# Performance work log

Hardware: AMD Instinct MI355X
Metric: run time of the kernel (lower is better)

Reference implementation:

```python
import jax, jax.numpy as jnp
import numpy as np

N, B, D_IN, D_OUT, E = 1024, 128, 64, 64, 16


def setup_inputs() -> dict:
    key = jax.random.key(0)
    k1, k2, k3, k4 = jax.random.split(key, 4)
    x = jax.random.normal(k1, (B, N, D_IN), dtype=jnp.float32)
    node_embeddings = jax.random.normal(k2, (N, E), dtype=jnp.float32)
    weights_pool = jax.random.normal(k3, (E, D_IN, D_OUT), dtype=jnp.float32)
    bias_pool = jax.random.normal(k4, (E, D_OUT), dtype=jnp.float32)
    return {"x": x, "node_embeddings": node_embeddings,
            "weights_pool": weights_pool, "bias_pool": bias_pool}


def reference(x, node_embeddings, weights_pool, bias_pool):
    # Adaptive adjacency: softmax over rows of relu(E E^T), shape [N, N]
    scores = jax.nn.relu(node_embeddings @ node_embeddings.T)
    supports = jax.nn.softmax(scores, axis=1)
    # Per-node weights [N, D_IN, D_OUT] and bias [N, D_OUT]
    weights = jnp.einsum('nd,dio->nio', node_embeddings, weights_pool)
    bias = node_embeddings @ bias_pool  # [N, D_OUT]
    # Graph aggregation: [B, N, D_IN]
    x_g = jnp.einsum('nm,bmc->bnc', supports, x)
    # Per-node linear transform + bias: [B, N, D_OUT]
    x_gconv = jnp.einsum('bni,nio->bno', x_g, weights) + bias
    return x_gconv
```

## Files before the change

kernel.cpp:

```cpp
#include <hip/hip_runtime.h>

#define N_NODES 1024
#define BATCH   128
#define E_DIM   16


typedef __attribute__((ext_vector_type(8))) short bf16x8;
typedef __attribute__((ext_vector_type(4))) float f32x4;
typedef __attribute__((ext_vector_type(16))) float f32x16;

__device__ __forceinline__ unsigned short f2bf(float f) {
    union { float f; unsigned int u; } v; v.f = f;
    unsigned int u = v.u;
    u += 0x7FFFu + ((u >> 16) & 1u);
    return (unsigned short)(u >> 16);
}

__device__ __forceinline__ void gload_lds16(const void* g, void* l) {
    __builtin_amdgcn_global_load_lds(
        (const __attribute__((address_space(1))) unsigned int*)g,
        (__attribute__((address_space(3))) unsigned int*)l, 16, 0, 0);
}

__global__ __launch_bounds__(256) void k_xt(const float* __restrict__ x,
                                            unsigned short* __restrict__ xbt) {
    const int bid = blockIdx.x;
    const int t = threadIdx.x;
    const int b = bid >> 4, kt64 = bid & 15;
    unsigned short* dstp = xbt + (long)(b >> 1) * 131072 + kt64 * 8192
                         + (b & 1) * 512;
#pragma unroll
    for (int h = 0; h < 2; ++h) {
        const int g = h * 256 + t;
        const int kblk = g >> 6, c = g & 63;
        const float* s = x + ((long)b * 1024 + kt64 * 64 + kblk * 8) * 64 + c;
        bf16x8 r;
#pragma unroll
        for (int e = 0; e < 8; ++e) r[e] = (short)f2bf(s[e * 64]);
        *(bf16x8*)(dstp + kblk * 1024 + c * 8) = r;
    }
}

__global__ __launch_bounds__(256) void k_wsup(const float* __restrict__ emb,
                                              const float* __restrict__ wpool,
                                              const float* __restrict__ bpool,
                                              unsigned short* __restrict__ sup,
                                              unsigned short* __restrict__ Wt,
                                              float* __restrict__ bias) {
    __shared__ float sm[132];
    const int bid = blockIdx.x;
    const int t = threadIdx.x;

    if (bid < 256) {
        float (*en4)[E_DIM] = (float(*)[E_DIM])sm;
        const int n0 = bid * 4;
        if (t < 64) en4[t >> 4][t & 15] = emb[(n0 + (t >> 4)) * E_DIM + (t & 15)];
        __syncthreads();
        const int o = t & 63;
#pragma unroll
        for (int p = 0; p < 2; ++p) {
            const int kblk = p * 4 + (t >> 6);
            float w[4][8];
#pragma unroll
            for (int nn = 0; nn < 4; ++nn)
#pragma unroll
                for (int e = 0; e < 8; ++e) w[nn][e] = 0.f;
            for (int ed = 0; ed < E_DIM; ++ed) {
                float v[8];
#pragma unroll
                for (int e = 0; e < 8; ++e)
                    v[e] = wpool[ed * 4096 + (kblk * 8 + e) * 64 + o];
#pragma unroll
                for (int nn = 0; nn < 4; ++nn)
#pragma unroll
                    for (int e = 0; e < 8; ++e)
                        w[nn][e] = fmaf(en4[nn][ed], v[e], w[nn][e]);
            }
#pragma unroll
            for (int nn = 0; nn < 4; ++nn) {
                bf16x8 r;
#pragma unroll
                for (int e = 0; e < 8; ++e) r[e] = (short)f2bf(w[nn][e]);
                *(bf16x8*)(Wt + (long)(n0 + nn) * 4096 + kblk * 512 + o * 8) = r;
            }
        }
        {
            const int nn = t >> 6, oo = t & 63;
            float s = 0.f;
#pragma unroll
            for (int e = 0; e < E_DIM; ++e) s = fmaf(en4[nn][e], bpool[e * 64 + oo], s);
            bias[(n0 + nn) * 64 + oo] = s;
        }
    } else {
        float* en  = sm;
        float* red = sm + 128;
        const int n = bid - 256;
        if (t < E_DIM) en[t] = emb[n * E_DIM + t];
        __syncthreads();
        float sc[4];
        float mx = -1e30f;
#pragma unroll
        for (int r = 0; r < 4; ++r) {
            const float* em = &emb[(r * 256 + t) * E_DIM];
            float s = 0.f;
#pragma unroll
            for (int e = 0; e < E_DIM; ++e) s = fmaf(en[e], em[e], s);
            s = fmaxf(s, 0.f);
            sc[r] = s;
            mx = fmaxf(mx, s);
        }
#pragma unroll
        for (int o = 32; o > 0; o >>= 1) mx = fmaxf(mx, __shfl_xor(mx, o));
        if ((t & 63) == 0) red[t >> 6] = mx;
        __syncthreads();
        mx = fmaxf(fmaxf(red[0], red[1]), fmaxf(red[2], red[3]));
        float sum = 0.f;
#pragma unroll
        for (int r = 0; r < 4; ++r) { sc[r] = __expf(sc[r] - mx); sum += sc[r]; }
#pragma unroll
        for (int o = 32; o > 0; o >>= 1) sum += __shfl_xor(sum, o);
        __syncthreads();
        if ((t & 63) == 0) red[t >> 6] = sum;
        __syncthreads();
        sum = red[0] + red[1] + red[2] + red[3];
        const float inv = 1.f / sum;
#pragma unroll
        for (int r = 0; r < 4; ++r) {
            const int m = r * 256 + t;
            const int off = (n >> 7) * 131072 + (m >> 6) * 8192 + ((m >> 3) & 7) * 1024
                          + (n & 127) * 8 + (m & 7);
            sup[off] = f2bf(sc[r] * inv);
        }
    }
}

__global__ __launch_bounds__(256, 3) void k_agg(const unsigned short* __restrict__ S,
                                                const unsigned short* __restrict__ Bt,
                                                unsigned short* __restrict__ xg) {
    __shared__ __align__(16) char lds[49152];
    const int t = threadIdx.x;
    const int lane = t & 63, wid = t >> 6;

    const int hw   = blockIdx.x + 8 * blockIdx.y;
    const int work = (hw & 7) * 64 + (hw >> 3);
    const int n0 = (work & 7) * 128, j0 = (work >> 3) * 128;
    const int wr = wid >> 1, wc = wid & 1;

    f32x16 acc[2][2];
#pragma unroll
    for (int m = 0; m < 2; ++m)
#pragma unroll
        for (int n = 0; n < 2; ++n)
#pragma unroll
            for (int r = 0; r < 16; ++r) acc[m][n][r] = 0.f;

    const unsigned short* pA = S  + (n0 >> 7) * 131072 + lane * 8;
    const unsigned short* pB = Bt + (j0 >> 7) * 131072 + lane * 8;
    const unsigned short* sp[4];
    int doff[4];
#pragma unroll
    for (int i = 0; i < 4; ++i) {
        const int c = wid * 4 + i;
        if (c < 8) { sp[i] = pA + c * 512;       doff[i] = c * 1024; }
        else       { sp[i] = pB + (c - 8) * 512; doff[i] = 8192 + (c - 8) * 1024; }
    }
#define STAGE(bufidx, kt) do {                                           \
        char* buf_ = lds + (bufidx) * 16384;                             \
        const int ko_ = (kt) * 4096;                                     \
        gload_lds16(sp[0] + ko_, buf_ + doff[0]);                        \
        gload_lds16(sp[1] + ko_, buf_ + doff[1]);                        \
        gload_lds16(sp[2] + ko_, buf_ + doff[2]);                        \
        gload_lds16(sp[3] + ko_, buf_ + doff[3]);                        \
    } while (0)

    int aoff[2], boff[2];
#pragma unroll
    for (int m = 0; m < 2; ++m)
        aoff[m] = (lane >> 5) * 2048 + (wr * 64 + m * 32 + (lane & 31)) * 16;
#pragma unroll
    for (int n = 0; n < 2; ++n)
        boff[n] = 8192 + (lane >> 5) * 2048 + (wc * 64 + n * 32 + (lane & 31)) * 16;

    STAGE(0, 0); STAGE(1, 1);
    int bcur = 0;
    for (int kt = 0; kt < 32; ++kt) {
        if (kt < 31) asm volatile("s_waitcnt vmcnt(4)" ::: "memory");
        else         asm volatile("s_waitcnt vmcnt(0)" ::: "memory");
        __builtin_amdgcn_s_barrier();
        asm volatile("" ::: "memory");
        __builtin_amdgcn_sched_barrier(0);
        const int bprev = (bcur + 2 >= 3) ? bcur - 1 : bcur + 2;
        if (kt + 2 < 32) STAGE(bprev, kt + 2);
        const char* cur = lds + bcur * 16384;
        __builtin_amdgcn_s_setprio(1);
#pragma unroll
        for (int s = 0; s < 2; ++s) {
            bf16x8 a[2], b[2];
#pragma unroll
            for (int m = 0; m < 2; ++m) a[m] = *(const bf16x8*)(cur + s * 4096 + aoff[m]);
#pragma unroll
            for (int n = 0; n < 2; ++n) b[n] = *(const bf16x8*)(cur + s * 4096 + boff[n]);
#pragma unroll
            for (int m = 0; m < 2; ++m)
#pragma unroll
                for (int n = 0; n < 2; ++n)
                    acc[m][n] = __builtin_amdgcn_mfma_f32_32x32x16_bf16(a[m], b[n], acc[m][n], 0, 0, 0);
        }
        __builtin_amdgcn_s_setprio(0);
        asm volatile("" ::: "memory");
        __builtin_amdgcn_sched_barrier(0);
        bcur = (bcur + 1 >= 3) ? 0 : bcur + 1;
    }
#undef STAGE
    __syncthreads();

    char* lb = lds;
#pragma unroll
    for (int m = 0; m < 2; ++m) {
#pragma unroll
        for (int n = 0; n < 2; ++n) {
            const int col  = wc * 64 + n * 32 + (lane & 31);
            const int rowb = wr * 64 + m * 32 + 4 * (lane >> 5);
#pragma unroll
            for (int r = 0; r < 16; ++r) {
                const int row = rowb + (r & 3) + 8 * (r >> 2);
                *(unsigned short*)(lb + row * 256 + ((col * 2) ^ ((row & 7) << 4))) =
                    f2bf(acc[m][n][r]);
            }
        }
    }
    __syncthreads();
    const int b0 = j0 >> 6;
#pragma unroll
    for (int i = 0; i < 8; ++i) {
        const int idx = i * 256 + t;
        const int row = idx >> 4, cc = idx & 15;
        bf16x8 v = *(const bf16x8*)(lb + row * 256 + ((cc * 16) ^ ((row & 7) << 4)));
        const int b = b0 + (cc >> 3);
        const long dst = (long)(n0 + row) * 8192 + b * 64 + ((cc & 7) ^ (b & 7)) * 8;
        *(bf16x8*)(xg + dst) = v;
    }
}

__global__ __launch_bounds__(256) void k_out(const unsigned short* __restrict__ xg,
                                             const unsigned short* __restrict__ Wt,
                                             const float* __restrict__ bias,
                                             float* __restrict__ out) {
    __shared__ __align__(16) char lds[49152];
    const int t = threadIdx.x, lane = t & 63, wid = t >> 6;
    const int nb = blockIdx.x * 2;
#pragma unroll
    for (int i = 0; i < 12; ++i) {
        const int c = wid * 12 + i;
        if (c < 32) {
            const int nn = c >> 4, k = c & 15;
            gload_lds16(xg + (long)(nb + nn) * 8192 + k * 512 + lane * 8,
                        lds + nn * 16384 + k * 1024);
        } else {
            const int cc = c - 32, nn = cc >> 3, k = cc & 7;
            gload_lds16(Wt + (long)(nb + nn) * 4096 + k * 512 + lane * 8,
                        lds + 32768 + nn * 8192 + k * 1024);
        }
    }
    __syncthreads();

    const int node = nb + (wid >> 1);
    const int bh   = wid & 1;
    const char* xl = lds + (wid >> 1) * 16384;
    const char* wlp = lds + 32768 + (wid >> 1) * 8192;

    f32x4 acc[4][4];
#pragma unroll
    for (int m = 0; m < 4; ++m)
#pragma unroll
        for (int n = 0; n < 4; ++n) acc[m][n] = f32x4{0.f, 0.f, 0.f, 0.f};

#pragma unroll
    for (int s = 0; s < 2; ++s) {
        const int kb = s * 4 + (lane >> 4);
        bf16x8 a[4], b[4];
#pragma unroll
        for (int m = 0; m < 4; ++m) {
            const int brow = bh * 64 + m * 16 + (lane & 15);
            a[m] = *(const bf16x8*)(xl + brow * 128 + ((kb ^ (lane & 7)) << 4));
        }
#pragma unroll
        for (int n = 0; n < 4; ++n)
            b[n] = *(const bf16x8*)(wlp + kb * 1024 + (n * 16 + (lane & 15)) * 16);
#pragma unroll
        for (int m = 0; m < 4; ++m)
#pragma unroll
            for (int n = 0; n < 4; ++n)
                acc[m][n] = __builtin_amdgcn_mfma_f32_16x16x32_bf16(a[m], b[n], acc[m][n], 0, 0, 0);
    }

#pragma unroll
    for (int n = 0; n < 4; ++n) {
        const int o = n * 16 + (lane & 15);
        const float bv = bias[node * 64 + o];
#pragma unroll
        for (int m = 0; m < 4; ++m) {
            const int b0 = bh * 64 + m * 16 + (lane >> 4) * 4;
#pragma unroll
            for (int r = 0; r < 4; ++r)
                out[(long)(b0 + r) * 65536 + node * 64 + o] = acc[m][n][r] + bv;
        }
    }
}

extern "C" void kernel_launch(void* const* d_in, const int* in_sizes, int n_in,
                              void* d_out, int out_size, void* d_ws, size_t ws_size,
                              hipStream_t stream) {
    const float* x     = (const float*)d_in[0];
    const float* emb   = (const float*)d_in[1];
    const float* wpool = (const float*)d_in[2];
    const float* bpool = (const float*)d_in[3];
    float* out = (float*)d_out;

    char* ws = (char*)d_ws;
    unsigned short* sup  = (unsigned short*)(ws);
    unsigned short* xbt  = (unsigned short*)(ws + (2u  << 20));
    unsigned short* Wt   = (unsigned short*)(ws + (18u << 20));
    float*          bias = (float*)         (ws + (26u << 20));
    unsigned short* xg   = (unsigned short*)(ws + (27u << 20));
    (void)in_sizes; (void)n_in; (void)out_size; (void)ws_size;

    k_xt<<<dim3(2048), dim3(256), 0, stream>>>(x, xbt);
    k_wsup<<<dim3(1280), dim3(256), 0, stream>>>(emb, wpool, bpool, sup, Wt, bias);
    k_agg<<<dim3(8, 64), dim3(256), 0, stream>>>(sup, xbt, xg);
    k_out<<<dim3(512), dim3(256), 0, stream>>>(xg, Wt, bias, out);
}
```

Baseline: 57.02 us.

## Merge prep kernels into one launch and stage output through LDS for vectorized stores

The x-transpose kernel and the weight/support prep kernel are combined into one launch, with block ranges dispatching the role. This removes a kernel launch and the gap between the two prep steps. The output kernel now writes its accumulators into a padded LDS tile in two passes and then issues coalesced 16-byte float4 global stores, replacing scattered 4-byte stores. In exchange it adds extra LDS traffic and several block barriers.

```diff
diff --git a/kernel.cpp b/kernel.cpp
--- a/kernel.cpp
+++ b/kernel.cpp
@@ -22,38 +22,35 @@
         (__attribute__((address_space(3))) unsigned int*)l, 16, 0, 0);
 }
 
-__global__ __launch_bounds__(256) void k_xt(const float* __restrict__ x,
-                                            unsigned short* __restrict__ xbt) {
-    const int bid = blockIdx.x;
-    const int t = threadIdx.x;
-    const int b = bid >> 4, kt64 = bid & 15;
-    unsigned short* dstp = xbt + (long)(b >> 1) * 131072 + kt64 * 8192
-                         + (b & 1) * 512;
-#pragma unroll
-    for (int h = 0; h < 2; ++h) {
-        const int g = h * 256 + t;
-        const int kblk = g >> 6, c = g & 63;
-        const float* s = x + ((long)b * 1024 + kt64 * 64 + kblk * 8) * 64 + c;
-        bf16x8 r;
-#pragma unroll
-        for (int e = 0; e < 8; ++e) r[e] = (short)f2bf(s[e * 64]);
-        *(bf16x8*)(dstp + kblk * 1024 + c * 8) = r;
-    }
-}
-
-__global__ __launch_bounds__(256) void k_wsup(const float* __restrict__ emb,
-                                              const float* __restrict__ wpool,
-                                              const float* __restrict__ bpool,
-                                              unsigned short* __restrict__ sup,
-                                              unsigned short* __restrict__ Wt,
-                                              float* __restrict__ bias) {
+__global__ __launch_bounds__(256) void k_prep2(const float* __restrict__ x,
+                                               const float* __restrict__ emb,
+                                               const float* __restrict__ wpool,
+                                               const float* __restrict__ bpool,
+                                               unsigned short* __restrict__ xbt,
+                                               unsigned short* __restrict__ sup,
+                                               unsigned short* __restrict__ Wt,
+                                               float* __restrict__ bias) {
     __shared__ float sm[132];
     const int bid = blockIdx.x;
     const int t = threadIdx.x;
 
-    if (bid < 256) {
+    if (bid < 2048) {
+        const int b = bid >> 4, kt64 = bid & 15;
+        unsigned short* dstp = xbt + (long)(b >> 1) * 131072 + kt64 * 8192
+                             + (b & 1) * 512;
+#pragma unroll
+        for (int h = 0; h < 2; ++h) {
+            const int g = h * 256 + t;
+            const int kblk = g >> 6, c = g & 63;
+            const float* s = x + ((long)b * 1024 + kt64 * 64 + kblk * 8) * 64 + c;
+            bf16x8 r;
+#pragma unroll
+            for (int e = 0; e < 8; ++e) r[e] = (short)f2bf(s[e * 64]);
+            *(bf16x8*)(dstp + kblk * 1024 + c * 8) = r;
+        }
+    } else if (bid < 2304) {
         float (*en4)[E_DIM] = (float(*)[E_DIM])sm;
-        const int n0 = bid * 4;
+        const int n0 = (bid - 2048) * 4;
         if (t < 64) en4[t >> 4][t & 15] = emb[(n0 + (t >> 4)) * E_DIM + (t & 15)];
         __syncthreads();
         const int o = t & 63;
@@ -94,7 +91,7 @@
     } else {
         float* en  = sm;
         float* red = sm + 128;
-        const int n = bid - 256;
+        const int n = bid - 2304;
         if (t < E_DIM) en[t] = emb[n * E_DIM + t];
         __syncthreads();
         float sc[4];
@@ -264,10 +261,12 @@
     }
     __syncthreads();
 
-    const int node = nb + (wid >> 1);
+    const int ns   = wid >> 1;
+    const int node = nb + ns;
     const int bh   = wid & 1;
-    const char* xl = lds + (wid >> 1) * 16384;
-    const char* wlp = lds + 32768 + (wid >> 1) * 8192;
+    const char* xl  = lds + ns * 16384;
+    const char* wlp = lds + 32768 + ns * 8192;
+    const int p = lane & 15, q = lane >> 4;
 
     f32x4 acc[4][4];
 #pragma unroll
@@ -277,16 +276,16 @@
 
 #pragma unroll
     for (int s = 0; s < 2; ++s) {
-        const int kb = s * 4 + (lane >> 4);
+        const int kb = s * 4 + q;
         bf16x8 a[4], b[4];
 #pragma unroll
         for (int m = 0; m < 4; ++m) {
-            const int brow = bh * 64 + m * 16 + (lane & 15);
+            const int brow = bh * 64 + m * 16 + p;
             a[m] = *(const bf16x8*)(xl + brow * 128 + ((kb ^ (lane & 7)) << 4));
         }
 #pragma unroll
         for (int n = 0; n < 4; ++n)
-            b[n] = *(const bf16x8*)(wlp + kb * 1024 + (n * 16 + (lane & 15)) * 16);
+            b[n] = *(const bf16x8*)(wlp + kb * 1024 + (n * 16 + p) * 16);
 #pragma unroll
         for (int m = 0; m < 4; ++m)
 #pragma unroll
@@ -294,17 +293,36 @@
                 acc[m][n] = __builtin_amdgcn_mfma_f32_16x16x32_bf16(a[m], b[n], acc[m][n], 0, 0, 0);
     }
 
-#pragma unroll
-    for (int n = 0; n < 4; ++n) {
-        const int o = n * 16 + (lane & 15);
-        const float bv = bias[node * 64 + o];
-#pragma unroll
-        for (int m = 0; m < 4; ++m) {
-            const int b0 = bh * 64 + m * 16 + (lane >> 4) * 4;
-#pragma unroll
-            for (int r = 0; r < 4; ++r)
-                out[(long)(b0 + r) * 65536 + node * 64 + o] = acc[m][n][r] + bv;
-        }
+    float bv[4];
+#pragma unroll
+    for (int n = 0; n < 4; ++n) bv[n] = bias[node * 64 + n * 16 + p];
+    __syncthreads();
+
+#pragma unroll
+    for (int pass = 0; pass < 2; ++pass) {
+        if (bh == pass) {
+            char* tb = lds + ns * 17408;
+#pragma unroll
+            for (int m = 0; m < 4; ++m)
+#pragma unroll
+                for (int n = 0; n < 4; ++n)
+#pragma unroll
+                    for (int r = 0; r < 4; ++r) {
+                        const int brow = m * 16 + q * 4 + r;
+                        *(float*)(tb + brow * 272 + (n * 16 + p) * 4) =
+                            acc[m][n][r] + bv[n];
+                    }
+        }
+        __syncthreads();
+#pragma unroll
+        for (int i = 0; i < 8; ++i) {
+            const int idx = i * 256 + t;
+            const int tns = idx >> 10, rem = idx & 1023;
+            const int b = rem >> 4, g = rem & 15;
+            f32x4 v = *(const f32x4*)(lds + tns * 17408 + b * 272 + g * 16);
+            *(f32x4*)(out + (long)(pass * 64 + b) * 65536 + (nb + tns) * 64 + g * 4) = v;
+        }
+        __syncthreads();
     }
 }
 
@@ -325,8 +343,8 @@
     unsigned short* xg   = (unsigned short*)(ws + (27u << 20));
     (void)in_sizes; (void)n_in; (void)out_size; (void)ws_size;
 
-    k_xt<<<dim3(2048), dim3(256), 0, stream>>>(x, xbt);
-    k_wsup<<<dim3(1280), dim3(256), 0, stream>>>(emb, wpool, bpool, sup, Wt, bias);
+    k_prep2<<<dim3(3328), dim3(256), 0, stream>>>(x, emb, wpool, bpool,
+                                                  xbt, sup, Wt, bias);
     k_agg<<<dim3(8, 64), dim3(256), 0, stream>>>(sup, xbt, xg);
     k_out<<<dim3(512), dim3(256), 0, stream>>>(xg, Wt, bias, out);
 }
```

Result: faster. 55.51 us (median of 2 runs) (-2.7%).
